# Performance work log

Hardware: AMD Instinct MI355X
Metric: run time of the kernel (lower is better)

The kernel has to match this reference:

```python
import jax, jax.numpy as jnp
import numpy as np

C_ATOM = 512
N_HEADS = 8
HEAD_DIM = C_ATOM // N_HEADS
N_ATOMS = 4
EPS = 1e-5


def _layernorm(x, g, b):
    mu = jnp.mean(x, axis=-1, keepdims=True)
    var = jnp.mean((x - mu) ** 2, axis=-1, keepdims=True)
    return (x - mu) * jax.lax.rsqrt(var + EPS) * g + b


def setup_inputs() -> dict:
    key = jax.random.key(0)
    ks = jax.random.split(key, 12)
    B, L = 2, 512
    s = 0.02
    inp = {
        "atom_feats": jax.random.normal(ks[0], (B, L, N_ATOMS, C_ATOM), jnp.float32),
        "mask": jnp.ones((B, L), dtype=bool),
        "ln1_g": jnp.ones((C_ATOM,), jnp.float32),
        "ln1_b": jnp.zeros((C_ATOM,), jnp.float32),
        "Wq": jax.random.normal(ks[1], (C_ATOM, C_ATOM), jnp.float32) * s,
        "bq": jnp.zeros((C_ATOM,), jnp.float32),
        "Wk": jax.random.normal(ks[2], (C_ATOM, C_ATOM), jnp.float32) * s,
        "bk": jnp.zeros((C_ATOM,), jnp.float32),
        "Wv": jax.random.normal(ks[3], (C_ATOM, C_ATOM), jnp.float32) * s,
        "bv": jnp.zeros((C_ATOM,), jnp.float32),
        "Wo": jax.random.normal(ks[4], (C_ATOM, C_ATOM), jnp.float32) * s,
        "bo": jnp.zeros((C_ATOM,), jnp.float32),
        "pair_bias": jax.random.normal(ks[5], (N_HEADS, N_ATOMS, N_ATOMS), jnp.float32) * 0.1,
        "ln2_g": jnp.ones((C_ATOM,), jnp.float32),
        "ln2_b": jnp.zeros((C_ATOM,), jnp.float32),
        "W1": jax.random.normal(ks[6], (4 * C_ATOM, C_ATOM), jnp.float32) * s,
        "b1": jnp.zeros((4 * C_ATOM,), jnp.float32),
        "W2": jax.random.normal(ks[7], (C_ATOM, 4 * C_ATOM), jnp.float32) * s,
        "b2": jnp.zeros((C_ATOM,), jnp.float32),
    }
    return inp


def reference(atom_feats, mask, ln1_g, ln1_b, Wq, bq, Wk, bk, Wv, bv, Wo, bo,
              pair_bias, ln2_g, ln2_b, W1, b1, W2, b2):
    B, L, n_atoms, C = atom_feats.shape
    S = L * n_atoms
    scale = HEAD_DIM ** (-0.5)
    x = atom_feats.reshape(B, S, C)
    h = _layernorm(x, ln1_g, ln1_b)
    # torch Linear: y = h @ W.T + b; split heads -> [B, H, S, D]
    q = (h @ Wq.T + bq).reshape(B, S, N_HEADS, HEAD_DIM).transpose(0, 2, 1, 3)
    k = (h @ Wk.T + bk).reshape(B, S, N_HEADS, HEAD_DIM).transpose(0, 2, 1, 3)
    v = (h @ Wv.T + bv).reshape(B, S, N_HEADS, HEAD_DIM).transpose(0, 2, 1, 3)
    attn = jnp.einsum('bhqd,bhkd->bhqk', q, k) * scale
    # periodic pair bias: bias[h, i, j] = pair_bias[h, i % 4, j % 4]
    bias = jnp.tile(pair_bias, (1, L, L))  # [H, S, S]
    attn = attn + bias[None]
    atom_mask = jnp.repeat(mask, n_atoms, axis=1)  # [B, S]
    attn = jnp.where(atom_mask[:, None, None, :], attn, -jnp.inf)
    attn = jax.nn.softmax(attn, axis=-1)
    out = jnp.einsum('bhqk,bhkd->bhqd', attn, v)
    out = out.transpose(0, 2, 1, 3).reshape(B, S, C)
    out = out @ Wo.T + bo
    x = x + out
    h2 = _layernorm(x, ln2_g, ln2_b)
    ff = jax.nn.gelu(h2 @ W1.T + b1, approximate=False) @ W2.T + b2
    x = x + ff
    return x.reshape(B, L, n_atoms, C)
```

## Files before the change

kernel.cpp:

```cpp
#include <hip/hip_runtime.h>
#include <cstdint>

typedef unsigned short u16;
typedef __attribute__((ext_vector_type(8))) short s16x8;
typedef __attribute__((ext_vector_type(4))) short s16x4;
typedef __attribute__((ext_vector_type(4))) float f32x4;
typedef __attribute__((ext_vector_type(2))) unsigned int u32x2;

#define SWZ(row, kb) ((kb) ^ (((row) & 7) << 4))

__device__ __forceinline__ u16 f2bf(float f) {
  unsigned u = __float_as_uint(f);
  u += 0x7FFFu + ((u >> 16) & 1u);
  return (u16)(u >> 16);
}

__device__ __forceinline__ unsigned cvt_pk_bf16(float lo, float hi) {
  unsigned r;
  asm("v_cvt_pk_bf16_f32 %0, %1, %2" : "=v"(r) : "v"(lo), "v"(hi));
  return r;
}

__device__ __forceinline__ float fast_exp2(float x) {
  float r;
  asm("v_exp_f32 %0, %1" : "=v"(r) : "v"(x));
  return r;
}

__device__ __forceinline__ float gelu_exact(float x) {
  const float s = x * 0.70710678118654752f;
  const float a = fabsf(s);
  const float t = __builtin_amdgcn_rcpf(1.f + 0.3275911f * a);
  float p = 1.061405429f;
  p = p * t - 1.453152027f;
  p = p * t + 1.421413741f;
  p = p * t - 0.284496736f;
  p = p * t + 0.254829592f;
  p = p * t;
  const float e = fast_exp2(a * a * -1.4426950408889634f);
  float er = 1.f - p * e;
  er = s < 0.f ? -er : er;
  return 0.5f * x * (1.f + er);
}

typedef __attribute__((address_space(3))) void lds_vp;
typedef __attribute__((address_space(1))) void gbl_vp;

__device__ __forceinline__ void gload_lds16(const void* g, void* l) {
  __builtin_amdgcn_global_load_lds((const gbl_vp*)(uintptr_t)g,
                                   (lds_vp*)(uint32_t)(uintptr_t)l, 16, 0, 0);
}

template <int RB>
__device__ __forceinline__ s16x8 lds_fragT(const char* base, int row, int kb) {
  return *(const s16x8*)(base + row * RB + ((kb) ^ (((row) & 7) << 4)));
}

__device__ __forceinline__ s16x8 lds_frag(const char* base, int row, int kb) {
  return lds_fragT<128>(base, row, kb);
}

template <int NROWS>
__device__ __forceinline__ void stage_tile(const u16* __restrict__ src, int stride,
                                           char* ldst, int t) {
#pragma unroll
  for (int j = 0; j < NROWS / 32; ++j) {
    int row = j * 32 + (t >> 3);
    int scb = SWZ(row, (t & 7) * 16);
    gload_lds16((const char*)(src + (size_t)row * stride) + scb,
                ldst + j * 4096 + (t & 192) * 16);
  }
}

template <int NROWS>
__device__ __forceinline__ void stage_tile8w(const u16* __restrict__ src, int stride,
                                             char* ldst, int t) {
#pragma unroll
  for (int j = 0; j < NROWS / 64; ++j) {
    int row = j * 64 + (t >> 3);
    int scb = SWZ(row, (t & 7) * 16);
    gload_lds16((const char*)(src + (size_t)row * stride) + scb,
                ldst + j * 8192 + (t >> 6) * 1024);
  }
}

template <int NROWS>
__device__ __forceinline__ void stage_t128_8w(const u16* __restrict__ src, int stride,
                                              char* ldst, int t) {
#pragma unroll
  for (int j = 0; j < NROWS / 32; ++j) {
    int row = j * 32 + (t >> 4);
    int scb = ((t & 15) * 16) ^ ((row & 7) << 4);
    gload_lds16((const char*)(src + (size_t)row * stride) + scb,
                ldst + j * 8192 + (t >> 6) * 1024);
  }
}

__global__ __launch_bounds__(256) void prep(const float* __restrict__ Wq,
                                            const float* __restrict__ Wk,
                                            const float* __restrict__ Wv,
                                            const float* __restrict__ Wo,
                                            const float* __restrict__ W1,
                                            const float* __restrict__ W2,
                                            u16* __restrict__ wqkv,
                                            u16* __restrict__ wob,
                                            u16* __restrict__ w1b,
                                            u16* __restrict__ w2b,
                                            const float* __restrict__ x,
                                            const float* __restrict__ gg,
                                            const float* __restrict__ bb,
                                            u16* __restrict__ out) {
  const int bid = (int)blockIdx.x;
  if (bid < 1536) {
    int i8 = bid * 256 + threadIdx.x;
    const float* s;
    u16* d;
    int off;
    if (i8 < 32768)       { s = Wq; d = wqkv;          off = i8; }
    else if (i8 < 65536)  { s = Wk; d = wqkv + 262144; off = i8 - 32768; }
    else if (i8 < 98304)  { s = Wv; d = wqkv + 524288; off = i8 - 65536; }
    else if (i8 < 131072) { s = Wo; d = wob;           off = i8 - 98304; }
    else if (i8 < 262144) { s = W1; d = w1b;           off = i8 - 131072; }
    else                  { s = W2; d = w2b;           off = i8 - 262144; }
    const float* sp = s + (size_t)off * 8;
    float4 a = *(const float4*)(sp);
    float4 b = *(const float4*)(sp + 4);
    s16x8 v;
    v[0] = (short)f2bf(a.x); v[1] = (short)f2bf(a.y);
    v[2] = (short)f2bf(a.z); v[3] = (short)f2bf(a.w);
    v[4] = (short)f2bf(b.x); v[5] = (short)f2bf(b.y);
    v[6] = (short)f2bf(b.z); v[7] = (short)f2bf(b.w);
    *(s16x8*)(d + (size_t)off * 8) = v;
  } else {
    int row = (bid - 1536) * 4 + (threadIdx.x >> 6);
    int l = threadIdx.x & 63;
    const float* xr = x + (size_t)row * 512;
    float v[8];
    float4 a = *(const float4*)(xr + l * 8);
    float4 c = *(const float4*)(xr + l * 8 + 4);
    v[0] = a.x; v[1] = a.y; v[2] = a.z; v[3] = a.w;
    v[4] = c.x; v[5] = c.y; v[6] = c.z; v[7] = c.w;
    float s = 0.f, q = 0.f;
#pragma unroll
    for (int i = 0; i < 8; ++i) { s += v[i]; q += v[i] * v[i]; }
#pragma unroll
    for (int sh = 1; sh < 64; sh <<= 1) {
      s += __shfl_xor(s, sh);
      q += __shfl_xor(q, sh);
    }
    float mu = s * (1.f / 512.f);
    float rs = rsqrtf(q * (1.f / 512.f) - mu * mu + 1e-5f);
    s16x8 o;
#pragma unroll
    for (int i = 0; i < 8; ++i) {
      int cc = l * 8 + i;
      o[i] = (short)f2bf((v[i] - mu) * rs * gg[cc] + bb[cc]);
    }
    *(s16x8*)(out + (size_t)row * 512 + l * 8) = o;
  }
}

__global__ __launch_bounds__(256) void ln_fwd(const float* __restrict__ x,
                                              const float* __restrict__ gg,
                                              const float* __restrict__ bb,
                                              u16* __restrict__ out) {
  int row = blockIdx.x * 4 + (threadIdx.x >> 6);
  int l = threadIdx.x & 63;
  const float* xr = x + (size_t)row * 512;
  float v[8];
  float4 a = *(const float4*)(xr + l * 8);
  float4 c = *(const float4*)(xr + l * 8 + 4);
  v[0] = a.x; v[1] = a.y; v[2] = a.z; v[3] = a.w;
  v[4] = c.x; v[5] = c.y; v[6] = c.z; v[7] = c.w;
  float s = 0.f, q = 0.f;
#pragma unroll
  for (int i = 0; i < 8; ++i) { s += v[i]; q += v[i] * v[i]; }
#pragma unroll
  for (int sh = 1; sh < 64; sh <<= 1) {
    s += __shfl_xor(s, sh);
    q += __shfl_xor(q, sh);
  }
  float mu = s * (1.f / 512.f);
  float rs = rsqrtf(q * (1.f / 512.f) - mu * mu + 1e-5f);
  s16x8 o;
#pragma unroll
  for (int i = 0; i < 8; ++i) {
    int cc = l * 8 + i;
    o[i] = (short)f2bf((v[i] - mu) * rs * gg[cc] + bb[cc]);
  }
  *(s16x8*)(out + (size_t)row * 512 + l * 8) = o;
}

template <int BM, int BN, int BK, int EPI>
__global__ __launch_bounds__(512, 4) void gemm2(const u16* __restrict__ A,
                                                const u16* __restrict__ Bt,
                                                const float* __restrict__ b0,
                                                const float* __restrict__ b1,
                                                const float* __restrict__ b2,
                                                const float* __restrict__ resid,
                                                void* __restrict__ o0,
                                                void* __restrict__ o1,
                                                void* __restrict__ o2,
                                                int M, int N, int K) {
  constexpr int MF = BM / 32;
  constexpr int NF = BN / 64;
  constexpr int RB = BK * 2;
  constexpr int HB = (BM + BN) * RB;
  constexpr int KC = BK / 32;
  __shared__ char lds[2 * HB];
  const int t = threadIdx.x, l = t & 63, w = t >> 6, g = l >> 4, ln = l & 15;
  const int wm = w >> 2, wn = w & 3;

  const int nyb = N / BN;
  const int nwg = (int)gridDim.x;
  const int bid = (int)blockIdx.x;
  const int swz = (bid & 7) * (nwg >> 3) + (bid >> 3);
  const int bm = (swz / nyb) * BM, bn = (swz % nyb) * BN;

  const u16* Ab = A + (size_t)bm * K;
  const u16* Bb = Bt + (size_t)bn * K;

  const f32x4 zz = {0.f, 0.f, 0.f, 0.f};
  f32x4 acc[MF][NF];
#pragma unroll
  for (int i = 0; i < MF; ++i)
#pragma unroll
    for (int j = 0; j < NF; ++j) acc[i][j] = zz;

  const int nt = K / BK;
  if constexpr (BK == 64) {
    stage_tile8w<BM>(Ab, K, lds, t);
    stage_tile8w<BN>(Bb, K, lds + BM * RB, t);
  } else {
    stage_t128_8w<BM>(Ab, K, lds, t);
    stage_t128_8w<BN>(Bb, K, lds + BM * RB, t);
  }
  asm volatile("s_waitcnt vmcnt(0)" ::: "memory");
  __syncthreads();

  int cur = 0;
  for (int tt = 0; tt < nt; ++tt) {
    const char* As = lds + cur * HB;
    const char* Bs = As + BM * RB;
    if (tt + 1 < nt) {
      char* An = lds + (cur ^ 1) * HB;
      if constexpr (BK == 64) {
        stage_tile8w<BM>(Ab + (tt + 1) * BK, K, An, t);
        stage_tile8w<BN>(Bb + (tt + 1) * BK, K, An + BM * RB, t);
      } else {
        stage_t128_8w<BM>(Ab + (tt + 1) * BK, K, An, t);
        stage_t128_8w<BN>(Bb + (tt + 1) * BK, K, An + BM * RB, t);
      }
    }
#pragma unroll
    for (int kk = 0; kk < KC; ++kk) {
      s16x8 af[MF], bfr[NF];
#pragma unroll
      for (int mf = 0; mf < MF; ++mf)
        af[mf] = lds_fragT<RB>(As, wm * (BM / 2) + mf * 16 + ln, kk * 64 + g * 16);
#pragma unroll
      for (int nf = 0; nf < NF; ++nf)
        bfr[nf] = lds_fragT<RB>(Bs, wn * (BN / 4) + nf * 16 + ln, kk * 64 + g * 16);
#pragma unroll
      for (int mf = 0; mf < MF; ++mf)
#pragma unroll
        for (int nf = 0; nf < NF; ++nf)
          acc[mf][nf] = __builtin_amdgcn_mfma_f32_16x16x32_bf16(af[mf], bfr[nf],
                                                                acc[mf][nf], 0, 0, 0);
    }
    if (tt + 1 < nt) {
      asm volatile("s_waitcnt vmcnt(0)" ::: "memory");
      __syncthreads();
    }
    cur ^= 1;
  }

#pragma unroll
  for (int mf = 0; mf < MF; ++mf)
#pragma unroll
    for (int nf = 0; nf < NF; ++nf) {
      const int col = bn + wn * (BN / 4) + nf * 16 + ln;
#pragma unroll
      for (int r = 0; r < 4; ++r) {
        const int row = bm + wm * (BM / 2) + mf * 16 + g * 4 + r;
        float v = acc[mf][nf][r];
        if constexpr (EPI == 1) {
          if (col < 512) {
            ((u16*)o0)[(size_t)row * 512 + col] =
                f2bf((v + b0[col]) * 0.18033688011112042f);
          } else if (col < 1024) {
            ((u16*)o1)[(size_t)row * 512 + (col - 512)] = f2bf(v + b1[col - 512]);
          } else {
            const int c2 = col - 1024;
            const int bi = row >> 11, s2 = row & 2047;
            ((u16*)o2)[((size_t)((bi * 8 + (c2 >> 6)) * 64 + (c2 & 63))) * 2048 + s2] =
                f2bf(v + b2[c2]);
          }
        } else if constexpr (EPI == 2) {
          ((u16*)o0)[(size_t)row * N + col] = f2bf(gelu_exact(v + b0[col]));
        } else {
          const float x = v + b0[col];
          ((float*)o0)[(size_t)row * N + col] = x + resid[(size_t)row * N + col];
        }
      }
    }
}

__global__ __launch_bounds__(512, 2) void attn2(const u16* __restrict__ qb,
                                                const u16* __restrict__ kb,
                                                const u16* __restrict__ vt,
                                                const float* __restrict__ pbias,
                                                u16* __restrict__ ob) {
  __shared__ char lds[81920];
  const int t = threadIdx.x, l = t & 63, g = l >> 4, ln = l & 15, w = t >> 6;
  const int sp = w >> 2, wg = w & 3, tg = t & 255;
  char* Ks0 = lds + sp * 32768;
  char* Vs0 = Ks0 + 16384;
  char* myP = lds + 65536 + w * 2048;

  const int qt = blockIdx.x, h = blockIdx.y, b = blockIdx.z;
  const int q0 = qt * 64 + wg * 16;
  const size_t rq = (size_t)(b * 2048 + q0);

  s16x8 qa[2];
#pragma unroll
  for (int kk = 0; kk < 2; ++kk)
    qa[kk] = *(const s16x8*)(qb + (rq + ln) * 512 + h * 64 + kk * 32 + g * 8);

  const float L2E = 1.4426950408889634f;
  float pbv[4];
#pragma unroll
  for (int r = 0; r < 4; ++r) pbv[r] = pbias[h * 16 + (l & 3) * 4 + r] * L2E;

  float mr = 0.f, lr = 0.f;
  const f32x4 zz = {0.f, 0.f, 0.f, 0.f};
  f32x4 oacc[4];
#pragma unroll
  for (int df = 0; df < 4; ++df) oacc[df] = zz;

  const u16* ks = kb + ((size_t)b * 2048) * 512 + h * 64;
  const u16* vs = vt + ((size_t)((b * 8 + h) * 64)) * 2048;

  const int it0 = sp * 16, itN = it0 + 16;
  stage_tile<64>(ks + (size_t)it0 * 64 * 512, 512, Ks0, tg);
  stage_tile<64>(vs + it0 * 64, 2048, Vs0, tg);
  asm volatile("s_waitcnt vmcnt(0)" ::: "memory");
  __syncthreads();

  int cur = 0;
  for (int it = it0; it < itN; ++it) {
    const char* Kc = Ks0 + cur * 8192;
    const char* Vc = Vs0 + cur * 8192;
    if (it + 1 < itN) {
      stage_tile<64>(ks + (size_t)(it + 1) * 64 * 512, 512, Ks0 + (cur ^ 1) * 8192, tg);
      stage_tile<64>(vs + (it + 1) * 64, 2048, Vs0 + (cur ^ 1) * 8192, tg);
    }

    f32x4 ini;
#pragma unroll
    for (int r = 0; r < 4; ++r) ini[r] = pbv[r] - mr;
    f32x4 sacc[4];
#pragma unroll
    for (int nf = 0; nf < 4; ++nf) sacc[nf] = ini;
#pragma unroll
    for (int kk = 0; kk < 2; ++kk) {
      s16x8 kf[4];
#pragma unroll
      for (int nf = 0; nf < 4; ++nf)
        kf[nf] = lds_frag(Kc, nf * 16 + ln, kk * 64 + g * 16);
      __builtin_amdgcn_s_setprio(1);
#pragma unroll
      for (int nf = 0; nf < 4; ++nf)
        sacc[nf] = __builtin_amdgcn_mfma_f32_16x16x32_bf16(kf[nf], qa[kk],
                                                           sacc[nf], 0, 0, 0);
      __builtin_amdgcn_s_setprio(0);
    }

    float m0 = fmaxf(fmaxf(sacc[0][0], sacc[0][1]), fmaxf(sacc[0][2], sacc[0][3]));
    float m1 = fmaxf(fmaxf(sacc[1][0], sacc[1][1]), fmaxf(sacc[1][2], sacc[1][3]));
    float m2 = fmaxf(fmaxf(sacc[2][0], sacc[2][1]), fmaxf(sacc[2][2], sacc[2][3]));
    float m3 = fmaxf(fmaxf(sacc[3][0], sacc[3][1]), fmaxf(sacc[3][2], sacc[3][3]));
    float lm = fmaxf(fmaxf(m0, m1), fmaxf(m2, m3));
    if (__any(lm > 8.f)) {
      float tm = fmaxf(lm, __shfl_xor(lm, 16));
      tm = fmaxf(tm, __shfl_xor(tm, 32));
      float al = fast_exp2(-tm);
      mr += tm;
      lr *= al;
      float alr[4];
#pragma unroll
      for (int r = 0; r < 4; ++r) alr[r] = __shfl(al, g * 4 + r);
#pragma unroll
      for (int df = 0; df < 4; ++df)
#pragma unroll
        for (int r = 0; r < 4; ++r) oacc[df][r] *= alr[r];
#pragma unroll
      for (int nf = 0; nf < 4; ++nf)
#pragma unroll
        for (int r = 0; r < 4; ++r) sacc[nf][r] -= tm;
    }

#pragma unroll
    for (int nf = 0; nf < 4; ++nf) {
      float p0 = fast_exp2(sacc[nf][0]);
      float p1 = fast_exp2(sacc[nf][1]);
      float p2 = fast_exp2(sacc[nf][2]);
      float p3 = fast_exp2(sacc[nf][3]);
      lr += (p0 + p1) + (p2 + p3);
      u32x2 pw;
      pw[0] = cvt_pk_bf16(p0, p1);
      pw[1] = cvt_pk_bf16(p2, p3);
      *(u32x2*)(myP + ln * 128 + ((nf * 32 + g * 8) ^ ((ln & 7) << 4))) = pw;
    }
    asm volatile("s_waitcnt lgkmcnt(0)" ::: "memory");
    __builtin_amdgcn_sched_barrier(0);

#pragma unroll
    for (int kk = 0; kk < 2; ++kk) {
      s16x8 pa, vf[4];
      pa = *(const s16x8*)(myP + ln * 128 + SWZ(ln, kk * 64 + g * 16));
#pragma unroll
      for (int df = 0; df < 4; ++df)
        vf[df] = lds_frag(Vc, df * 16 + ln, kk * 64 + g * 16);
      __builtin_amdgcn_s_setprio(1);
#pragma unroll
      for (int df = 0; df < 4; ++df)
        oacc[df] = __builtin_amdgcn_mfma_f32_16x16x32_bf16(pa, vf[df],
                                                           oacc[df], 0, 0, 0);
      __builtin_amdgcn_s_setprio(0);
    }

    if (it + 1 < itN) {
      asm volatile("s_waitcnt vmcnt(0)" ::: "memory");
      __syncthreads();
    }
    cur ^= 1;
  }

  lr += __shfl_xor(lr, 16);
  lr += __shfl_xor(lr, 32);

  float* cb = (float*)lds + wg * (16 * 65 + 32);
  __syncthreads();
  if (sp == 1) {
    if (l < 16) {
      cb[16 * 65 + l] = mr;
      cb[16 * 65 + 16 + l] = lr;
    }
#pragma unroll
    for (int df = 0; df < 4; ++df)
#pragma unroll
      for (int r = 0; r < 4; ++r)
        cb[(g * 4 + r) * 65 + df * 16 + ln] = oacc[df][r];
  }
  __syncthreads();
  if (sp == 0) {
    float m1 = cb[16 * 65 + ln], l1 = cb[16 * 65 + 16 + ln];
    float M = fmaxf(mr, m1);
    float e0 = fast_exp2(mr - M), e1 = fast_exp2(m1 - M);
    float inv = 1.f / (lr * e0 + l1 * e1);
    float w0 = e0 * inv, w1 = e1 * inv;
    float w0q[4], w1q[4];
#pragma unroll
    for (int r = 0; r < 4; ++r) {
      w0q[r] = __shfl(w0, g * 4 + r);
      w1q[r] = __shfl(w1, g * 4 + r);
    }
#pragma unroll
    for (int df = 0; df < 4; ++df)
#pragma unroll
      for (int r = 0; r < 4; ++r) {
        float o = oacc[df][r] * w0q[r] + cb[(g * 4 + r) * 65 + df * 16 + ln] * w1q[r];
        ob[(rq + g * 4 + r) * 512 + h * 64 + df * 16 + ln] = f2bf(o);
      }
  }
}

extern "C" void kernel_launch(void* const* d_in, const int* in_sizes, int n_in,
                              void* d_out, int out_size, void* d_ws, size_t ws_size,
                              hipStream_t stream) {
  const float* atom = (const float*)d_in[0];
  const float* ln1g = (const float*)d_in[2];
  const float* ln1b = (const float*)d_in[3];
  const float* Wq = (const float*)d_in[4];  const float* bq = (const float*)d_in[5];
  const float* Wk = (const float*)d_in[6];  const float* bk = (const float*)d_in[7];
  const float* Wv = (const float*)d_in[8];  const float* bv = (const float*)d_in[9];
  const float* Wo = (const float*)d_in[10]; const float* bo = (const float*)d_in[11];
  const float* pb = (const float*)d_in[12];
  const float* ln2g = (const float*)d_in[13];
  const float* ln2b = (const float*)d_in[14];
  const float* W1 = (const float*)d_in[15]; const float* b1 = (const float*)d_in[16];
  const float* W2 = (const float*)d_in[17]; const float* b2 = (const float*)d_in[18];
  float* out = (float*)d_out;

  char* ws = (char*)d_ws;
  u16* h1 = (u16*)(ws + ((size_t)0 << 20));
  u16* qb = (u16*)(ws + ((size_t)4 << 20));
  u16* kb = (u16*)(ws + ((size_t)8 << 20));
  u16* vt = (u16*)(ws + ((size_t)12 << 20));
  u16* ao = (u16*)(ws + ((size_t)16 << 20));
  float* x1 = (float*)(ws + ((size_t)20 << 20));
  u16* h2 = (u16*)(ws + ((size_t)28 << 20));
  u16* ff = (u16*)(ws + ((size_t)32 << 20));
  u16* wqkv = (u16*)(ws + ((size_t)48 << 20));
  u16* wob = (u16*)(ws + ((size_t)49 << 20) + (512 << 10));
  u16* w1b = (u16*)(ws + ((size_t)50 << 20));
  u16* w2b = (u16*)(ws + ((size_t)52 << 20));

  prep<<<dim3(2560), 256, 0, stream>>>(Wq, Wk, Wv, Wo, W1, W2, wqkv, wob, w1b, w2b,
                                       atom, ln1g, ln1b, h1);

  gemm2<64, 128, 64, 1><<<dim3(768), 512, 0, stream>>>(h1, wqkv, bq, bk, bv, nullptr,
                                                       qb, kb, vt, 4096, 1536, 512);

  attn2<<<dim3(32, 8, 2), 512, 0, stream>>>(qb, kb, vt, pb, ao);

  gemm2<64, 64, 128, 3><<<dim3(512), 512, 0, stream>>>(ao, wob, bo, nullptr, nullptr,
                                                       atom, x1, nullptr, nullptr,
                                                       4096, 512, 512);

  ln_fwd<<<dim3(1024), 256, 0, stream>>>(x1, ln2g, ln2b, h2);

  gemm2<64, 256, 64, 2><<<dim3(512), 512, 0, stream>>>(h2, w1b, b1, nullptr, nullptr,
                                                       nullptr, ff, nullptr, nullptr,
                                                       4096, 2048, 512);

  gemm2<64, 64, 128, 3><<<dim3(512), 512, 0, stream>>>(ff, w2b, b2, nullptr, nullptr,
                                                       x1, out, nullptr, nullptr,
                                                       4096, 512, 2048);
}
```

Before: 97.35 us.

## Fold LayerNorm2 into Wo epilogue stats and W1 GEMM algebra

Result: slower. 104.4 us (+7.2%).

```diff
diff --git a/kernel.cpp b/kernel.cpp
--- a/kernel.cpp
+++ b/kernel.cpp
@@ -109,29 +109,43 @@
                                             const float* __restrict__ x,
                                             const float* __restrict__ gg,
                                             const float* __restrict__ bb,
-                                            u16* __restrict__ out) {
+                                            u16* __restrict__ out,
+                                            const float* __restrict__ g2,
+                                            const float* __restrict__ b2,
+                                            const float* __restrict__ b1,
+                                            float* __restrict__ uu,
+                                            float* __restrict__ v1b,
+                                            float* __restrict__ stats) {
   const int bid = (int)blockIdx.x;
   if (bid < 1536) {
     int i8 = bid * 256 + threadIdx.x;
     const float* s;
     u16* d;
     int off;
+    bool isW1 = false;
     if (i8 < 32768)       { s = Wq; d = wqkv;          off = i8; }
     else if (i8 < 65536)  { s = Wk; d = wqkv + 262144; off = i8 - 32768; }
     else if (i8 < 98304)  { s = Wv; d = wqkv + 524288; off = i8 - 65536; }
     else if (i8 < 131072) { s = Wo; d = wob;           off = i8 - 98304; }
-    else if (i8 < 262144) { s = W1; d = w1b;           off = i8 - 131072; }
+    else if (i8 < 262144) { s = W1; d = w1b;           off = i8 - 131072; isW1 = true; }
     else                  { s = W2; d = w2b;           off = i8 - 262144; }
     const float* sp = s + (size_t)off * 8;
     float4 a = *(const float4*)(sp);
     float4 b = *(const float4*)(sp + 4);
+    if (isW1) {
+      const float* gp = g2 + ((off & 63) * 8);
+      float4 ga = *(const float4*)(gp);
+      float4 gb = *(const float4*)(gp + 4);
+      a.x *= ga.x; a.y *= ga.y; a.z *= ga.z; a.w *= ga.w;
+      b.x *= gb.x; b.y *= gb.y; b.z *= gb.z; b.w *= gb.w;
+    }
     s16x8 v;
     v[0] = (short)f2bf(a.x); v[1] = (short)f2bf(a.y);
     v[2] = (short)f2bf(a.z); v[3] = (short)f2bf(a.w);
     v[4] = (short)f2bf(b.x); v[5] = (short)f2bf(b.y);
     v[6] = (short)f2bf(b.z); v[7] = (short)f2bf(b.w);
     *(s16x8*)(d + (size_t)off * 8) = v;
-  } else {
+  } else if (bid < 2560) {
     int row = (bid - 1536) * 4 + (threadIdx.x >> 6);
     int l = threadIdx.x & 63;
     const float* xr = x + (size_t)row * 512;
@@ -157,38 +171,37 @@
       o[i] = (short)f2bf((v[i] - mu) * rs * gg[cc] + bb[cc]);
     }
     *(s16x8*)(out + (size_t)row * 512 + l * 8) = o;
-  }
-}
-
-__global__ __launch_bounds__(256) void ln_fwd(const float* __restrict__ x,
-                                              const float* __restrict__ gg,
-                                              const float* __restrict__ bb,
-                                              u16* __restrict__ out) {
-  int row = blockIdx.x * 4 + (threadIdx.x >> 6);
-  int l = threadIdx.x & 63;
-  const float* xr = x + (size_t)row * 512;
-  float v[8];
-  float4 a = *(const float4*)(xr + l * 8);
-  float4 c = *(const float4*)(xr + l * 8 + 4);
-  v[0] = a.x; v[1] = a.y; v[2] = a.z; v[3] = a.w;
-  v[4] = c.x; v[5] = c.y; v[6] = c.z; v[7] = c.w;
-  float s = 0.f, q = 0.f;
-#pragma unroll
-  for (int i = 0; i < 8; ++i) { s += v[i]; q += v[i] * v[i]; }
-#pragma unroll
-  for (int sh = 1; sh < 64; sh <<= 1) {
-    s += __shfl_xor(s, sh);
-    q += __shfl_xor(q, sh);
-  }
-  float mu = s * (1.f / 512.f);
-  float rs = rsqrtf(q * (1.f / 512.f) - mu * mu + 1e-5f);
-  s16x8 o;
-#pragma unroll
-  for (int i = 0; i < 8; ++i) {
-    int cc = l * 8 + i;
-    o[i] = (short)f2bf((v[i] - mu) * rs * gg[cc] + bb[cc]);
-  }
-  *(s16x8*)(out + (size_t)row * 512 + l * 8) = o;
+  } else if (bid < 2564) {
+    int i = (bid - 2560) * 256 + threadIdx.x;
+#pragma unroll
+    for (int j = 0; j < 8; ++j) stats[i * 8 + j] = 0.f;
+  } else {
+    const int w = threadIdx.x >> 6, l = threadIdx.x & 63;
+    const int n0 = (bid - 2564) * 32 + w * 8;
+#pragma unroll
+    for (int i = 0; i < 8; ++i) {
+      const int n = n0 + i;
+      const float* wr = W1 + (size_t)n * 512 + l * 8;
+      const float* gp = g2 + l * 8;
+      const float* bp = b2 + l * 8;
+      float su = 0.f, sv = 0.f;
+#pragma unroll
+      for (int j = 0; j < 8; ++j) {
+        const float wv = wr[j];
+        su += gp[j] * wv;
+        sv += bp[j] * wv;
+      }
+#pragma unroll
+      for (int sh = 1; sh < 64; sh <<= 1) {
+        su += __shfl_xor(su, sh);
+        sv += __shfl_xor(sv, sh);
+      }
+      if (l == 0) {
+        uu[n] = su;
+        v1b[n] = sv + b1[n];
+      }
+    }
+  }
 }
 
 template <int BM, int BN, int BK, int EPI>
@@ -275,35 +288,83 @@
     cur ^= 1;
   }
 
-#pragma unroll
-  for (int mf = 0; mf < MF; ++mf)
-#pragma unroll
-    for (int nf = 0; nf < NF; ++nf) {
-      const int col = bn + wn * (BN / 4) + nf * 16 + ln;
+  if constexpr (EPI == 5) {
+    float pv[MF][4], pq[MF][4];
+    const int col = bn + wn * 16 + ln;
+#pragma unroll
+    for (int mf = 0; mf < MF; ++mf)
 #pragma unroll
       for (int r = 0; r < 4; ++r) {
         const int row = bm + wm * (BM / 2) + mf * 16 + g * 4 + r;
-        float v = acc[mf][nf][r];
-        if constexpr (EPI == 1) {
-          if (col < 512) {
-            ((u16*)o0)[(size_t)row * 512 + col] =
-                f2bf((v + b0[col]) * 0.18033688011112042f);
-          } else if (col < 1024) {
-            ((u16*)o1)[(size_t)row * 512 + (col - 512)] = f2bf(v + b1[col - 512]);
+        float v = acc[mf][0][r] + b0[col] + resid[(size_t)row * N + col];
+        ((float*)o0)[(size_t)row * N + col] = v;
+        ((u16*)o1)[(size_t)row * N + col] = f2bf(v);
+        float vs = v * v;
+#pragma unroll
+        for (int sh = 1; sh < 16; sh <<= 1) {
+          v += __shfl_xor(v, sh);
+          vs += __shfl_xor(vs, sh);
+        }
+        pv[mf][r] = v;
+        pq[mf][r] = vs;
+      }
+    float* sA = (float*)lds;
+    float* qA = (float*)lds + 256;
+    __syncthreads();
+    if (ln == 0) {
+#pragma unroll
+      for (int mf = 0; mf < MF; ++mf)
+#pragma unroll
+        for (int r = 0; r < 4; ++r) {
+          const int rl = wm * (BM / 2) + mf * 16 + g * 4 + r;
+          sA[rl * 4 + wn] = pv[mf][r];
+          qA[rl * 4 + wn] = pq[mf][r];
+        }
+    }
+    __syncthreads();
+    if (t < 64) {
+      float s = sA[t * 4] + sA[t * 4 + 1] + sA[t * 4 + 2] + sA[t * 4 + 3];
+      float q = qA[t * 4] + qA[t * 4 + 1] + qA[t * 4 + 2] + qA[t * 4 + 3];
+      atomicAdd((float*)o2 + 2 * (bm + t), s);
+      atomicAdd((float*)o2 + 2 * (bm + t) + 1, q);
+    }
+  } else {
+#pragma unroll
+    for (int mf = 0; mf < MF; ++mf)
+#pragma unroll
+      for (int nf = 0; nf < NF; ++nf) {
+        const int col = bn + wn * (BN / 4) + nf * 16 + ln;
+#pragma unroll
+        for (int r = 0; r < 4; ++r) {
+          const int row = bm + wm * (BM / 2) + mf * 16 + g * 4 + r;
+          float v = acc[mf][nf][r];
+          if constexpr (EPI == 1) {
+            if (col < 512) {
+              ((u16*)o0)[(size_t)row * 512 + col] =
+                  f2bf((v + b0[col]) * 0.18033688011112042f);
+            } else if (col < 1024) {
+              ((u16*)o1)[(size_t)row * 512 + (col - 512)] = f2bf(v + b1[col - 512]);
+            } else {
+              const int c2 = col - 1024;
+              const int bi = row >> 11, s2 = row & 2047;
+              ((u16*)o2)[((size_t)((bi * 8 + (c2 >> 6)) * 64 + (c2 & 63))) * 2048 + s2] =
+                  f2bf(v + b2[c2]);
+            }
+          } else if constexpr (EPI == 2) {
+            ((u16*)o0)[(size_t)row * N + col] = f2bf(gelu_exact(v + b0[col]));
+          } else if constexpr (EPI == 4) {
+            const float s = b2[2 * row], q = b2[2 * row + 1];
+            const float mu = s * (1.f / 512.f);
+            const float rs = rsqrtf(q * (1.f / 512.f) - mu * mu + 1e-5f);
+            const float val = rs * (v - mu * b0[col]) + b1[col];
+            ((u16*)o0)[(size_t)row * N + col] = f2bf(gelu_exact(val));
           } else {
-            const int c2 = col - 1024;
-            const int bi = row >> 11, s2 = row & 2047;
-            ((u16*)o2)[((size_t)((bi * 8 + (c2 >> 6)) * 64 + (c2 & 63))) * 2048 + s2] =
-                f2bf(v + b2[c2]);
+            const float x = v + b0[col];
+            ((float*)o0)[(size_t)row * N + col] = x + resid[(size_t)row * N + col];
           }
-        } else if constexpr (EPI == 2) {
-          ((u16*)o0)[(size_t)row * N + col] = f2bf(gelu_exact(v + b0[col]));
-        } else {
-          const float x = v + b0[col];
-          ((float*)o0)[(size_t)row * N + col] = x + resid[(size_t)row * N + col];
         }
       }
-    }
+  }
 }
 
 __global__ __launch_bounds__(512, 2) void attn2(const u16* __restrict__ qb,
@@ -500,28 +561,30 @@
   u16* vt = (u16*)(ws + ((size_t)12 << 20));
   u16* ao = (u16*)(ws + ((size_t)16 << 20));
   float* x1 = (float*)(ws + ((size_t)20 << 20));
-  u16* h2 = (u16*)(ws + ((size_t)28 << 20));
+  u16* xb = (u16*)(ws + ((size_t)28 << 20));
   u16* ff = (u16*)(ws + ((size_t)32 << 20));
   u16* wqkv = (u16*)(ws + ((size_t)48 << 20));
   u16* wob = (u16*)(ws + ((size_t)49 << 20) + (512 << 10));
   u16* w1b = (u16*)(ws + ((size_t)50 << 20));
   u16* w2b = (u16*)(ws + ((size_t)52 << 20));
-
-  prep<<<dim3(2560), 256, 0, stream>>>(Wq, Wk, Wv, Wo, W1, W2, wqkv, wob, w1b, w2b,
-                                       atom, ln1g, ln1b, h1);
+  float* stats = (float*)(ws + ((size_t)54 << 20));
+  float* uu = (float*)(ws + ((size_t)54 << 20) + (64 << 10));
+  float* v1b = (float*)(ws + ((size_t)54 << 20) + (128 << 10));
+
+  prep<<<dim3(2628), 256, 0, stream>>>(Wq, Wk, Wv, Wo, W1, W2, wqkv, wob, w1b, w2b,
+                                       atom, ln1g, ln1b, h1, ln2g, ln2b, b1,
+                                       uu, v1b, stats);
 
   gemm2<64, 128, 64, 1><<<dim3(768), 512, 0, stream>>>(h1, wqkv, bq, bk, bv, nullptr,
                                                        qb, kb, vt, 4096, 1536, 512);
 
   attn2<<<dim3(32, 8, 2), 512, 0, stream>>>(qb, kb, vt, pb, ao);
 
-  gemm2<64, 64, 128, 3><<<dim3(512), 512, 0, stream>>>(ao, wob, bo, nullptr, nullptr,
-                                                       atom, x1, nullptr, nullptr,
+  gemm2<64, 64, 128, 5><<<dim3(512), 512, 0, stream>>>(ao, wob, bo, nullptr, nullptr,
+                                                       atom, x1, xb, stats,
                                                        4096, 512, 512);
 
-  ln_fwd<<<dim3(1024), 256, 0, stream>>>(x1, ln2g, ln2b, h2);
-
-  gemm2<64, 256, 64, 2><<<dim3(512), 512, 0, stream>>>(h2, w1b, b1, nullptr, nullptr,
+  gemm2<64, 256, 64, 4><<<dim3(512), 512, 0, stream>>>(xb, w1b, uu, v1b, stats,
                                                        nullptr, ff, nullptr, nullptr,
                                                        4096, 2048, 512);
 
```
